# Kernel tuning notes

Hardware: AMD Instinct MI355X
Metric: run time of the kernel (lower is better)

The kernel has to match this reference:

```python
import jax, jax.numpy as jnp
import numpy as np

B, NPG, HID, HEADS, L = 8, 512, 128, 8, 4
N = B * NPG
E = 16384
EDIM = HID // 4  # edge_dim = hidden_dim // 4 = 32


def _ln(x, g, b):
    m = x.mean(-1, keepdims=True)
    v = ((x - m) ** 2).mean(-1, keepdims=True)
    return (x - m) / jnp.sqrt(v + 1e-5) * g + b


def setup_inputs() -> dict:
    key = jax.random.key(0)
    ks = jax.random.split(key, 24)
    s = 0.05
    epg = E // B
    base = jnp.repeat(jnp.arange(B) * NPG, epg)
    src = base + jax.random.randint(ks[0], (E,), 0, NPG)
    dst = base + jax.random.randint(ks[1], (E,), 0, NPG)
    d = {
        'x': jax.random.randint(ks[2], (N, 1), 0, 100),
        'edge_index': jnp.stack([src, dst]),
        'edge_attr': jax.random.normal(ks[3], (E, 1), jnp.float32),
        'batch': jnp.repeat(jnp.arange(B), NPG),
        'atom_emb': jax.random.normal(ks[4], (100, HID)) * s,
        'edge_w': jax.random.normal(ks[5], (1, EDIM)) * s,
        'edge_b': jnp.zeros((EDIM,)),
        'wq': jax.random.normal(ks[6], (L, HID, HEADS * HID)) * s,
        'bq': jnp.zeros((L, HEADS * HID)),
        'wk': jax.random.normal(ks[7], (L, HID, HEADS * HID)) * s,
        'bk': jnp.zeros((L, HEADS * HID)),
        'wv': jax.random.normal(ks[8], (L, HID, HEADS * HID)) * s,
        'bv': jnp.zeros((L, HEADS * HID)),
        'we': jax.random.normal(ks[9], (L, EDIM, HEADS * HID)) * s,
        'wskip': jax.random.normal(ks[10], (L, HID, HID)) * s,
        'bskip': jnp.zeros((L, HID)),
        'ln_g': jnp.ones((L, HID)),
        'ln_b': jnp.zeros((L, HID)),
        'mha_in_w': jax.random.normal(ks[11], (HID, 3 * HID)) * s,
        'mha_in_b': jnp.zeros((3 * HID,)),
        'mha_out_w': jax.random.normal(ks[12], (HID, HID)) * s,
        'mha_out_b': jnp.zeros((HID,)),
        'w1': jax.random.normal(ks[13], (HID, HID)) * s,
        'b1': jnp.zeros((HID,)),
        'w2': jax.random.normal(ks[14], (HID, HID // 2)) * s,
        'b2': jnp.zeros((HID // 2,)),
        'w3': jax.random.normal(ks[15], (HID // 2, 3)) * s,
        'b3': jnp.zeros((3,)),
    }
    return d


def reference(x, edge_index, edge_attr, batch, atom_emb, edge_w, edge_b,
              wq, bq, wk, bk, wv, bv, we, wskip, bskip, ln_g, ln_b,
              mha_in_w, mha_in_b, mha_out_w, mha_out_b, w1, b1, w2, b2, w3, b3):
    src, dst = edge_index[0], edge_index[1]
    h = atom_emb[x[:, 0]]                       # [N, HID]
    e = edge_attr @ edge_w + edge_b             # [E, EDIM]
    scale = 1.0 / jnp.sqrt(jnp.float32(HID))    # per-head channel dim = HID
    for i in range(L):
        res = h
        q = (h @ wq[i] + bq[i]).reshape(N, HEADS, HID)
        k = (h @ wk[i] + bk[i]).reshape(N, HEADS, HID)
        v = (h @ wv[i] + bv[i]).reshape(N, HEADS, HID)
        ee = (e @ we[i]).reshape(E, HEADS, HID)
        kj = k[src] + ee                        # [E, HEADS, HID]
        vj = v[src] + ee
        logits = jnp.einsum('ehd,ehd->eh', q[dst], kj) * scale
        m = jax.ops.segment_max(logits, dst, num_segments=N)
        a = jnp.exp(logits - m[dst])
        z = jax.ops.segment_sum(a, dst, num_segments=N)
        a = a / (z[dst] + 1e-16)                # edge softmax per target node
        agg = jax.ops.segment_sum(a[:, :, None] * vj, dst, num_segments=N)
        out = agg.mean(axis=1) + h @ wskip[i] + bskip[i]  # concat=False + root skip
        h = jax.nn.gelu(_ln(out + res, ln_g[i], ln_b[i]), approximate=False)
    # equal-size graphs: ragged->padded conversion is a plain reshape, no padding
    p = h.reshape(B, NPG, HID)
    qkv = p @ mha_in_w + mha_in_b               # [B, n, 3*HID]
    hd = HID // HEADS
    q, k, v = [t.reshape(B, NPG, HEADS, hd).transpose(0, 2, 1, 3)
               for t in jnp.split(qkv, 3, axis=-1)]
    att = jax.nn.softmax(jnp.einsum('bhqd,bhkd->bhqk', q, k) / jnp.sqrt(jnp.float32(hd)), axis=-1)
    o = jnp.einsum('bhqk,bhkd->bhqd', att, v).transpose(0, 2, 1, 3).reshape(B, NPG, HID)
    o = (o @ mha_out_w + mha_out_b).reshape(N, HID)
    y = jax.nn.gelu(o @ w1 + b1, approximate=False)
    y = jax.nn.gelu(y @ w2 + b2, approximate=False)
    return y @ w3 + b3                          # [N, 3]
```

## Files before the change

kernel.cpp:

```cpp
#include <hip/hip_runtime.h>
#include <hip/hip_bf16.h>
#include <math.h>

#define NN 4096
#define NE 16384
#define NLAYERS 4

#define WT_STRIDE 442368

typedef __attribute__((ext_vector_type(8))) short bf16x8;
typedef __attribute__((ext_vector_type(4))) float floatx4;

__device__ __forceinline__ float gelu_f(float x) {
  return 0.5f * x * (1.0f + erff(x * 0.70710678118654752440f));
}

__device__ __forceinline__ void bsplit(float a, unsigned short& hi, unsigned short& lo) {
  __hip_bfloat16 h16 = __float2bfloat16(a);
  hi = *(unsigned short*)&h16;
  const float r = a - __bfloat162float(h16);
  __hip_bfloat16 l16 = __float2bfloat16(r);
  lo = *(unsigned short*)&l16;
}

union F16U { float4 v4[4]; float f[16]; };

__global__ void k_init(const int* __restrict__ x, const float* __restrict__ atom_emb,
                       const float* __restrict__ edge_attr, const float* __restrict__ edge_w,
                       const float* __restrict__ edge_b, float* __restrict__ h,
                       float* __restrict__ ef, int* __restrict__ counts,
                       unsigned short* __restrict__ hhi, unsigned short* __restrict__ hlo) {
  const int idx = blockIdx.x * 256 + threadIdx.x;
  const float hv = atom_emb[x[idx >> 7] * 128 + (idx & 127)];
  h[idx] = hv;
  bsplit(hv, hhi[idx], hlo[idx]);
  ef[idx] = edge_attr[idx >> 5] * edge_w[idx & 31] + edge_b[idx & 31];
  if (idx < NN) counts[idx] = 0;
}

__global__ void k_hist(const int* __restrict__ eidx, int* __restrict__ counts) {
  const int e = blockIdx.x * 256 + threadIdx.x;
  if (e < NE) atomicAdd(&counts[eidx[NE + e]], 1);
}

__global__ void k_scan2(const int* __restrict__ counts, int* __restrict__ offs,
                        const int* __restrict__ eidx, int* __restrict__ elist) {
  __shared__ int tmp[1024];
  __shared__ int sheads[4096];
  const int t = threadIdx.x;
  const int c0 = counts[t*4], c1 = counts[t*4+1], c2 = counts[t*4+2], c3 = counts[t*4+3];
  const int s = c0 + c1 + c2 + c3;
  tmp[t] = s; __syncthreads();
  for (int off = 1; off < 1024; off <<= 1) {
    int v = (t >= off) ? tmp[t - off] : 0;
    __syncthreads();
    tmp[t] += v;
    __syncthreads();
  }
  int base = tmp[t] - s;
  offs[t*4]   = base;                sheads[t*4]   = base;
  offs[t*4+1] = base + c0;           sheads[t*4+1] = base + c0;
  offs[t*4+2] = base + c0 + c1;      sheads[t*4+2] = base + c0 + c1;
  offs[t*4+3] = base + c0 + c1 + c2; sheads[t*4+3] = base + c0 + c1 + c2;
  if (t == 1023) offs[NN] = tmp[1023];
  __syncthreads();
  for (int e = t; e < NE; e += 1024) {
    const int p = atomicAdd(&sheads[eidx[NE + e]], 1);
    elist[p] = e;
  }
}

__global__ __launch_bounds__(256) void k_wcvt(
    const float* __restrict__ wq, const float* __restrict__ wk,
    const float* __restrict__ wv, const float* __restrict__ wsk,
    unsigned short* __restrict__ wthi, unsigned short* __restrict__ wtlo) {
  const int z = blockIdx.z;
  const int layer = z >> 2, mat = z & 3;
  int NC; const float* W; int woff;
  if (mat == 0)      { NC = 1024; W = wq  + (size_t)layer * 131072; woff = 0; }
  else if (mat == 1) { NC = 1024; W = wk  + (size_t)layer * 131072; woff = 131072; }
  else if (mat == 2) { NC = 1024; W = wv  + (size_t)layer * 131072; woff = 262144; }
  else               { NC = 128;  W = wsk + (size_t)layer * 16384;  woff = 393216; }
  const int c0 = blockIdx.x * 64;
  if (c0 >= NC) return;
  const int k0 = blockIdx.y * 64;
  __shared__ unsigned short th[64][65], tl[64][65];
  const int t = threadIdx.x;
  for (int i = t; i < 4096; i += 256) {
    const int kk = i >> 6, c = i & 63;
    bsplit(W[(size_t)(k0 + kk) * NC + c0 + c], th[kk][c], tl[kk][c]);
  }
  __syncthreads();
  unsigned short* oh = wthi + (size_t)layer * WT_STRIDE + woff;
  unsigned short* ol = wtlo + (size_t)layer * WT_STRIDE + woff;
  for (int i = t; i < 4096; i += 256) {
    const int n = i >> 6, k = i & 63;
    oh[(size_t)(c0 + n) * 128 + k0 + k] = th[k][n];
    ol[(size_t)(c0 + n) * 128 + k0 + k] = tl[k][n];
  }
}

__global__ __launch_bounds__(256) void k_wqe(
    const float* __restrict__ wq, const float* __restrict__ bq,
    const float* __restrict__ we, unsigned short* __restrict__ wthi,
    unsigned short* __restrict__ wtlo, float* __restrict__ bqe) {
  const int layer = blockIdx.x >> 3, hh = blockIdx.x & 7;
  const float* wq_l = wq + (size_t)layer * 131072;
  const float* we_l = we + (size_t)layer * 32768;
  const float* bq_l = bq + (size_t)layer * 1024;
  __shared__ float wqS[128][132];
  __shared__ float weS[32][132];
  const int t = threadIdx.x;
  for (int i = t; i < 4096; i += 256) {
    const int d = i >> 5, dd4 = (i & 31) << 2;
    *(float4*)&wqS[d][dd4] = *(const float4*)&wq_l[(size_t)d * 1024 + hh * 128 + dd4];
  }
  for (int i = t; i < 1024; i += 256) {
    const int c = i >> 5, dd4 = (i & 31) << 2;
    *(float4*)&weS[c][dd4] = *(const float4*)&we_l[(size_t)c * 1024 + hh * 128 + dd4];
  }
  __syncthreads();
  const int d = t & 127, cg = t >> 7;
  float acc[16];
  #pragma unroll
  for (int cc = 0; cc < 16; cc++) acc[cc] = 0.f;
  for (int dd = 0; dd < 128; dd++) {
    const float a = wqS[d][dd];
    #pragma unroll
    for (int cc = 0; cc < 16; cc++)
      acc[cc] += a * weS[cg * 16 + cc][dd];
  }
  unsigned short* oh = wthi + (size_t)layer * WT_STRIDE + 409600;
  unsigned short* ol = wtlo + (size_t)layer * WT_STRIDE + 409600;
  #pragma unroll
  for (int cc = 0; cc < 16; cc++) {
    const int j = hh * 32 + cg * 16 + cc;
    unsigned short hi, lo;
    bsplit(acc[cc], hi, lo);
    oh[(size_t)j * 128 + d] = hi;
    ol[(size_t)j * 128 + d] = lo;
  }
  if (t < 32) {
    float s = 0.f;
    for (int dd = 0; dd < 128; dd++) s += bq_l[hh * 128 + dd] * weS[t][dd];
    bqe[layer * 256 + hh * 32 + t] = s;
  }
}

__global__ __launch_bounds__(256) void k_mfqkv(
    const unsigned short* __restrict__ hhi, const unsigned short* __restrict__ hlo,
    const unsigned short* __restrict__ wth, const unsigned short* __restrict__ wtl,
    const float* __restrict__ bq, const float* __restrict__ bk,
    const float* __restrict__ bv, const float* __restrict__ bsk,
    const float* __restrict__ bqe_l,
    float* __restrict__ qb, float* __restrict__ kb,
    float* __restrict__ vb, float* __restrict__ skb, float* __restrict__ qeb) {
  const int xb = blockIdx.x;
  int NC; const float* bias; float* C; int woff; int c0;
  if (xb < 16)      { NC = 1024; bias = bq;    C = qb;  woff = 0;      c0 = xb * 64; }
  else if (xb < 32) { NC = 1024; bias = bk;    C = kb;  woff = 131072; c0 = (xb-16) * 64; }
  else if (xb < 48) { NC = 1024; bias = bv;    C = vb;  woff = 262144; c0 = (xb-32) * 64; }
  else if (xb < 50) { NC = 128;  bias = bsk;   C = skb; woff = 393216; c0 = (xb-48) * 64; }
  else              { NC = 256;  bias = bqe_l; C = qeb; woff = 409600; c0 = (xb-50) * 64; }
  __shared__ unsigned short Ah[64][136], Al[64][136], Wh[64][136], Wl[64][136];
  const int t = threadIdx.x;
  const int n0 = blockIdx.y * 64;
  for (int i = t; i < 1024; i += 256) {
    const int r = i >> 4, c8 = (i & 15) << 3;
    *(uint4*)&Ah[r][c8] = *(const uint4*)&hhi[(size_t)(n0 + r) * 128 + c8];
    *(uint4*)&Al[r][c8] = *(const uint4*)&hlo[(size_t)(n0 + r) * 128 + c8];
    *(uint4*)&Wh[r][c8] = *(const uint4*)&wth[woff + (size_t)(c0 + r) * 128 + c8];
    *(uint4*)&Wl[r][c8] = *(const uint4*)&wtl[woff + (size_t)(c0 + r) * 128 + c8];
  }
  __syncthreads();
  const int w = t >> 6, l = t & 63;
  const int quad = l >> 4, lm = l & 15;
  floatx4 acc[4] = {{0.f,0.f,0.f,0.f},{0.f,0.f,0.f,0.f},{0.f,0.f,0.f,0.f},{0.f,0.f,0.f,0.f}};
  #pragma unroll
  for (int kc = 0; kc < 4; kc++) {
    const int ko = kc * 32 + quad * 8;
    const bf16x8 ah = *(const bf16x8*)&Ah[w * 16 + lm][ko];
    const bf16x8 al = *(const bf16x8*)&Al[w * 16 + lm][ko];
    #pragma unroll
    for (int ct = 0; ct < 4; ct++) {
      const bf16x8 bh = *(const bf16x8*)&Wh[ct * 16 + lm][ko];
      const bf16x8 bl = *(const bf16x8*)&Wl[ct * 16 + lm][ko];
      acc[ct] = __builtin_amdgcn_mfma_f32_16x16x32_bf16(ah, bh, acc[ct], 0, 0, 0);
      acc[ct] = __builtin_amdgcn_mfma_f32_16x16x32_bf16(ah, bl, acc[ct], 0, 0, 0);
      acc[ct] = __builtin_amdgcn_mfma_f32_16x16x32_bf16(al, bh, acc[ct], 0, 0, 0);
    }
  }
  #pragma unroll
  for (int ct = 0; ct < 4; ct++) {
    const int col = c0 + ct * 16 + lm;
    const float bb = bias[col];
    #pragma unroll
    for (int r = 0; r < 4; r++) {
      const int row = n0 + w * 16 + quad * 4 + r;
      C[(size_t)row * NC + col] = acc[ct][r] + bb;
    }
  }
}

__global__ __launch_bounds__(256) void k_gemm2(const float* __restrict__ A,
                                               const float* __restrict__ W,
                                               const float* __restrict__ bias,
                                               float* __restrict__ C, int NC, int gelu) {
  __shared__ float As[128][65];
  __shared__ float Ws[128][64];
  const int t = threadIdx.x;
  const int n0 = blockIdx.y * 64, c0 = blockIdx.x * 64;
  for (int i = t; i < 2048; i += 256) {
    const int r = i & 63, k4 = (i >> 6) << 2;
    const float4 a = *(const float4*)&A[(size_t)(n0 + r) * 128 + k4];
    As[k4+0][r] = a.x; As[k4+1][r] = a.y; As[k4+2][r] = a.z; As[k4+3][r] = a.w;
  }
  for (int i = t; i < 2048; i += 256) {
    const int kk = i >> 4, c4 = (i & 15) << 2;
    *(float4*)&Ws[kk][c4] = *(const float4*)&W[(size_t)kk * NC + c0 + c4];
  }
  __syncthreads();
  const int tr = (t >> 4) << 2;
  const int tc = (t & 15) << 2;
  float acc[4][4];
  #pragma unroll
  for (int i = 0; i < 4; i++)
    #pragma unroll
    for (int j = 0; j < 4; j++) acc[i][j] = 0.f;
  #pragma unroll 8
  for (int k = 0; k < 128; k++) {
    const float4 av = *(const float4*)&As[k][tr];
    const float4 wv = *(const float4*)&Ws[k][tc];
    acc[0][0] += av.x*wv.x; acc[0][1] += av.x*wv.y; acc[0][2] += av.x*wv.z; acc[0][3] += av.x*wv.w;
    acc[1][0] += av.y*wv.x; acc[1][1] += av.y*wv.y; acc[1][2] += av.y*wv.z; acc[1][3] += av.y*wv.w;
    acc[2][0] += av.z*wv.x; acc[2][1] += av.z*wv.y; acc[2][2] += av.z*wv.z; acc[2][3] += av.z*wv.w;
    acc[3][0] += av.w*wv.x; acc[3][1] += av.w*wv.y; acc[3][2] += av.w*wv.z; acc[3][3] += av.w*wv.w;
  }
  const float4 bb = *(const float4*)&bias[c0 + tc];
  #pragma unroll
  for (int i = 0; i < 4; i++) {
    float4 v;
    v.x = acc[i][0] + bb.x; v.y = acc[i][1] + bb.y;
    v.z = acc[i][2] + bb.z; v.w = acc[i][3] + bb.w;
    if (gelu) { v.x = gelu_f(v.x); v.y = gelu_f(v.y); v.z = gelu_f(v.z); v.w = gelu_f(v.w); }
    *(float4*)&C[(size_t)(n0 + tr + i) * NC + c0 + tc] = v;
  }
}

__global__ __launch_bounds__(256) void k_edgepost(
    const float* __restrict__ qb, const float* __restrict__ kb,
    const float* __restrict__ vb, const float* __restrict__ qe,
    const float* __restrict__ ef, const int* __restrict__ offs,
    const int* __restrict__ elist, const int* __restrict__ eidx,
    const float* __restrict__ we_l, const float* __restrict__ skb,
    const float* __restrict__ lng, const float* __restrict__ lnb,
    float* __restrict__ h,
    unsigned short* __restrict__ hhi, unsigned short* __restrict__ hlo) {
  __shared__ float Ss[4][256];
  __shared__ float Am[4][128];
  const int t = threadIdx.x;
  const int wid = t >> 6, lane = t & 63;
  const int n0 = (blockIdx.x & 7) * 512 + (blockIdx.x >> 3) * 4;
  const int n = n0 + wid;
  {
    const int hh = lane >> 3, s8 = lane & 7;
    const int d0 = hh * 128 + s8 * 16;
    F16U qv;
    {
      const float4* qp = (const float4*)(qb + (size_t)n * 1024 + d0);
      #pragma unroll
      for (int i = 0; i < 4; i++) qv.v4[i] = qp[i];
    }
    const float4 qe4 = *(const float4*)(qe + (size_t)n * 256 + hh * 32 + s8 * 4);
    float m = -INFINITY, z = 0.f;
    float acc[16];
    #pragma unroll
    for (int i = 0; i < 16; i++) acc[i] = 0.f;
    float sx = 0.f, sy = 0.f, sz = 0.f, sw = 0.f;
    const int e0 = offs[n], e1 = offs[n + 1];
    int ecur = 0, scur = 0;
    if (e0 < e1) { ecur = elist[e0]; scur = eidx[ecur]; }
    for (int tt = e0; tt < e1; tt++) {
      F16U kv, vv;
      {
        const float4* kp = (const float4*)(kb + (size_t)scur * 1024 + d0);
        const float4* vp = (const float4*)(vb + (size_t)scur * 1024 + d0);
        #pragma unroll
        for (int i = 0; i < 4; i++) { kv.v4[i] = kp[i]; vv.v4[i] = vp[i]; }
      }
      const float4 ef4 = *(const float4*)(ef + (size_t)ecur * 32 + s8 * 4);
      if (tt + 1 < e1) { ecur = elist[tt + 1]; scur = eidx[ecur]; }
      float p0 = qe4.x*ef4.x + qe4.y*ef4.y;
      float p1 = qe4.z*ef4.z + qe4.w*ef4.w;
      float p2 = 0.f, p3 = 0.f;
      #pragma unroll
      for (int i = 0; i < 4; i++) {
        p0 += qv.f[i]      * kv.f[i];
        p1 += qv.f[4 + i]  * kv.f[4 + i];
        p2 += qv.f[8 + i]  * kv.f[8 + i];
        p3 += qv.f[12 + i] * kv.f[12 + i];
      }
      float p = (p0 + p1) + (p2 + p3);
      p += __shfl_xor(p, 1);
      p += __shfl_xor(p, 2);
      p += __shfl_xor(p, 4);
      const float logit = p * 0.08838834764831845f;
      if (logit > m + 8.f) {
        const float f = __expf(m - logit);
        z *= f; sx *= f; sy *= f; sz *= f; sw *= f;
        #pragma unroll
        for (int i = 0; i < 16; i++) acc[i] *= f;
        m = logit;
      }
      const float w = __expf(logit - m);
      z += w;
      #pragma unroll
      for (int i = 0; i < 16; i++) acc[i] += w * vv.f[i];
      sx += w * ef4.x; sy += w * ef4.y;
      sz += w * ef4.z; sw += w * ef4.w;
    }
    const float inv = 1.f / (z + 1e-16f);
    *(float4*)&Ss[wid][hh * 32 + s8 * 4] =
        make_float4(sx * inv, sy * inv, sz * inv, sw * inv);
    F16U ov;
    #pragma unroll
    for (int i = 0; i < 16; i++) ov.f[i] = acc[i] * inv;
    #pragma unroll
    for (int mask = 8; mask <= 32; mask <<= 1)
      #pragma unroll
      for (int i = 0; i < 16; i++) ov.f[i] += __shfl_xor(ov.f[i], mask);
    if (hh == 0) {
      #pragma unroll
      for (int i = 0; i < 16; i++) ov.f[i] *= 0.125f;
      #pragma unroll
      for (int i = 0; i < 4; i++)
        *(float4*)&Am[wid][s8 * 16 + i * 4] = ov.v4[i];
    }
  }
  {
    const int half = lane >> 5;
    const int q4 = (lane & 31) << 2;
    float ax = 0.f, ay = 0.f, az = 0.f, aw = 0.f;
    #pragma unroll 8
    for (int i = 0; i < 128; i++) {
      const int k = half * 128 + i;
      const float4 wv = *(const float4*)&we_l[(size_t)(k & 31) * 1024 + (k >> 5) * 128 + q4];
      const float s = Ss[wid][k];
      ax += s * wv.x; ay += s * wv.y; az += s * wv.z; aw += s * wv.w;
    }
    ax += __shfl_xor(ax, 32); ay += __shfl_xor(ay, 32);
    az += __shfl_xor(az, 32); aw += __shfl_xor(aw, 32);
    if (lane < 32) {
      const size_t o = (size_t)n * 128 + q4;
      const float4 sk4 = *(const float4*)&skb[o];
      const float4 h4  = *(const float4*)&h[o];
      float4 am = *(float4*)&Am[wid][q4];
      am.x += 0.125f * ax + sk4.x + h4.x;
      am.y += 0.125f * ay + sk4.y + h4.y;
      am.z += 0.125f * az + sk4.z + h4.z;
      am.w += 0.125f * aw + sk4.w + h4.w;
      *(float4*)&Am[wid][q4] = am;
    }
  }
  {
    const float v0 = Am[wid][lane], v1 = Am[wid][lane + 64];
    float s = v0 + v1;
    #pragma unroll
    for (int mask = 1; mask <= 32; mask <<= 1) s += __shfl_xor(s, mask);
    const float mean = s * (1.f / 128.f);
    const float d0 = v0 - mean, d1 = v1 - mean;
    float q = d0 * d0 + d1 * d1;
    #pragma unroll
    for (int mask = 1; mask <= 32; mask <<= 1) q += __shfl_xor(q, mask);
    const float rstd = 1.f / sqrtf(q * (1.f / 128.f) + 1e-5f);
    const float y0 = d0 * rstd * lng[lane] + lnb[lane];
    const float y1 = d1 * rstd * lng[lane + 64] + lnb[lane + 64];
    const float r0 = gelu_f(y0);
    const float r1 = gelu_f(y1);
    const size_t o = (size_t)n * 128 + lane;
    h[o] = r0;
    h[o + 64] = r1;
    bsplit(r0, hhi[o], hlo[o]);
    bsplit(r1, hhi[o + 64], hlo[o + 64]);
  }
}

__global__ __launch_bounds__(256) void k_attn2b(const float* __restrict__ qkvm,
                                                float* __restrict__ pm,
                                                float* __restrict__ pz,
                                                float* __restrict__ pacc) {
  __shared__ float ks2[64][16];
  __shared__ float vs2[64][16];
  const int ksp = blockIdx.x, qt = blockIdx.y, bh = blockIdx.z;
  const int b = bh >> 3, hh = bh & 7;
  const int t = threadIdx.x;
  const size_t rbase = (size_t)(b * 512 + ksp * 64);
  {
    const int j = t >> 2, d4 = (t & 3) << 2;
    const size_t ro = (rbase + j) * 384 + hh * 16 + d4;
    *(float4*)&ks2[j][d4] = *(const float4*)&qkvm[ro + 128];
    *(float4*)&vs2[j][d4] = *(const float4*)&qkvm[ro + 256];
  }
  __syncthreads();
  const int qrow = qt * 256 + t;
  const int nq = b * 512 + qrow;
  F16U qv;
  {
    const float4* qp = (const float4*)(qkvm + (size_t)nq * 384 + hh * 16);
    #pragma unroll
    for (int i = 0; i < 4; i++) qv.v4[i] = qp[i];
  }
  float m = -INFINITY, z = 0.f;
  float acc[16];
  #pragma unroll
  for (int i = 0; i < 16; i++) acc[i] = 0.f;
  for (int j = 0; j < 64; j += 2) {
    F16U k0, k1, v0, v1;
    {
      const float4* p0 = (const float4*)ks2[j];
      const float4* p1 = (const float4*)ks2[j + 1];
      const float4* q0 = (const float4*)vs2[j];
      const float4* q1 = (const float4*)vs2[j + 1];
      #pragma unroll
      for (int i = 0; i < 4; i++) {
        k0.v4[i] = p0[i]; k1.v4[i] = p1[i];
        v0.v4[i] = q0[i]; v1.v4[i] = q1[i];
      }
    }
    float a0 = 0.f, a1 = 0.f, a2 = 0.f, a3 = 0.f;
    float b0 = 0.f, b1 = 0.f, b2 = 0.f, b3 = 0.f;
    #pragma unroll
    for (int i = 0; i < 4; i++) {
      a0 += qv.f[i]      * k0.f[i];
      a1 += qv.f[4 + i]  * k0.f[4 + i];
      a2 += qv.f[8 + i]  * k0.f[8 + i];
      a3 += qv.f[12 + i] * k0.f[12 + i];
      b0 += qv.f[i]      * k1.f[i];
      b1 += qv.f[4 + i]  * k1.f[4 + i];
      b2 += qv.f[8 + i]  * k1.f[8 + i];
      b3 += qv.f[12 + i] * k1.f[12 + i];
    }
    const float sa = ((a0 + a1) + (a2 + a3)) * 0.25f;
    const float sb = ((b0 + b1) + (b2 + b3)) * 0.25f;
    const float smax = fmaxf(sa, sb);
    if (smax > m + 8.f) {
      const float f = __expf(m - smax);
      z *= f;
      #pragma unroll
      for (int i = 0; i < 16; i++) acc[i] *= f;
      m = smax;
    }
    const float wa = __expf(sa - m);
    const float wb = __expf(sb - m);
    z += wa + wb;
    #pragma unroll
    for (int i = 0; i < 16; i++)
      acc[i] += wa * v0.f[i] + wb * v1.f[i];
  }
  const int p = (bh * 512 + qrow) * 8 + ksp;
  pm[p] = m; pz[p] = z;
  float4* pp = (float4*)&pacc[(size_t)p * 16];
  F16U ov;
  #pragma unroll
  for (int i = 0; i < 16; i++) ov.f[i] = acc[i];
  #pragma unroll
  for (int i = 0; i < 4; i++) pp[i] = ov.v4[i];
}

__global__ __launch_bounds__(256) void k_tail(
    const float* __restrict__ pm, const float* __restrict__ pz,
    const float* __restrict__ pacc,
    const float* __restrict__ mow, const float* __restrict__ mob,
    const float* __restrict__ w1, const float* __restrict__ b1,
    const float* __restrict__ w2, const float* __restrict__ b2,
    const float* __restrict__ w3, const float* __restrict__ b3,
    float* __restrict__ out) {
  __shared__ float RA[8][128];
  __shared__ float RB[8][128];
  const int t = threadIdx.x;
  const int w = t >> 6, lane = t & 63;
  const int n0 = blockIdx.x * 8;
  const int rA = w * 2, rB = w * 2 + 1;
  #pragma unroll
  for (int rr = 0; rr < 2; rr++) {
    const int n = n0 + w * 2 + rr;
    const int b = n >> 9, qrow = n & 511;
    #pragma unroll
    for (int half = 0; half < 2; half++) {
      const int c = lane + half * 64;
      const int hh = c >> 4, d = c & 15;
      const int base = ((b * 8 + hh) * 512 + qrow) * 8;
      float ms = pm[base];
      #pragma unroll
      for (int s = 1; s < 8; s++) ms = fmaxf(ms, pm[base + s]);
      float z = 0.f, o = 0.f;
      #pragma unroll
      for (int s = 0; s < 8; s++) {
        const float wg = __expf(pm[base + s] - ms);
        z += pz[base + s] * wg;
        o += pacc[(size_t)(base + s) * 16 + d] * wg;
      }
      RA[w * 2 + rr][c] = o / z;
    }
  }
  {
    const int kk = lane >> 5;
    const int c4 = (lane & 31) << 2;
    float a0x=0.f,a0y=0.f,a0z=0.f,a0w=0.f, a1x=0.f,a1y=0.f,a1z=0.f,a1w=0.f;
    #pragma unroll 8
    for (int i = 0; i < 64; i++) {
      const int k = kk + (i << 1);
      const float4 wv = *(const float4*)&mow[(size_t)k * 128 + c4];
      const float r0 = RA[rA][k], r1 = RA[rB][k];
      a0x += r0*wv.x; a0y += r0*wv.y; a0z += r0*wv.z; a0w += r0*wv.w;
      a1x += r1*wv.x; a1y += r1*wv.y; a1z += r1*wv.z; a1w += r1*wv.w;
    }
    a0x += __shfl_xor(a0x, 32); a0y += __shfl_xor(a0y, 32);
    a0z += __shfl_xor(a0z, 32); a0w += __shfl_xor(a0w, 32);
    a1x += __shfl_xor(a1x, 32); a1y += __shfl_xor(a1y, 32);
    a1z += __shfl_xor(a1z, 32); a1w += __shfl_xor(a1w, 32);
    if (lane < 32) {
      RB[rA][c4+0] = a0x + mob[c4+0]; RB[rA][c4+1] = a0y + mob[c4+1];
      RB[rA][c4+2] = a0z + mob[c4+2]; RB[rA][c4+3] = a0w + mob[c4+3];
      RB[rB][c4+0] = a1x + mob[c4+0]; RB[rB][c4+1] = a1y + mob[c4+1];
      RB[rB][c4+2] = a1z + mob[c4+2]; RB[rB][c4+3] = a1w + mob[c4+3];
    }
  }
  {
    const int kk = lane >> 5;
    const int c4 = (lane & 31) << 2;
    float a0x=0.f,a0y=0.f,a0z=0.f,a0w=0.f, a1x=0.f,a1y=0.f,a1z=0.f,a1w=0.f;
    #pragma unroll 8
    for (int i = 0; i < 64; i++) {
      const int k = kk + (i << 1);
      const float4 wv = *(const float4*)&w1[(size_t)k * 128 + c4];
      const float r0 = RB[rA][k], r1 = RB[rB][k];
      a0x += r0*wv.x; a0y += r0*wv.y; a0z += r0*wv.z; a0w += r0*wv.w;
      a1x += r1*wv.x; a1y += r1*wv.y; a1z += r1*wv.z; a1w += r1*wv.w;
    }
    a0x += __shfl_xor(a0x, 32); a0y += __shfl_xor(a0y, 32);
    a0z += __shfl_xor(a0z, 32); a0w += __shfl_xor(a0w, 32);
    a1x += __shfl_xor(a1x, 32); a1y += __shfl_xor(a1y, 32);
    a1z += __shfl_xor(a1z, 32); a1w += __shfl_xor(a1w, 32);
    if (lane < 32) {
      RA[rA][c4+0] = gelu_f(a0x + b1[c4+0]); RA[rA][c4+1] = gelu_f(a0y + b1[c4+1]);
      RA[rA][c4+2] = gelu_f(a0z + b1[c4+2]); RA[rA][c4+3] = gelu_f(a0w + b1[c4+3]);
      RB[rA][c4+0] = 0.f;
      RA[rB][c4+0] = gelu_f(a1x + b1[c4+0]); RA[rB][c4+1] = gelu_f(a1y + b1[c4+1]);
      RA[rB][c4+2] = gelu_f(a1z + b1[c4+2]); RA[rB][c4+3] = gelu_f(a1w + b1[c4+3]);
    }
  }
  {
    const int kk = lane >> 4;
    const int c4 = (lane & 15) << 2;
    float a0x=0.f,a0y=0.f,a0z=0.f,a0w=0.f, a1x=0.f,a1y=0.f,a1z=0.f,a1w=0.f;
    #pragma unroll 8
    for (int i = 0; i < 32; i++) {
      const int k = kk + (i << 2);
      const float4 wv = *(const float4*)&w2[(size_t)k * 64 + c4];
      const float r0 = RA[rA][k], r1 = RA[rB][k];
      a0x += r0*wv.x; a0y += r0*wv.y; a0z += r0*wv.z; a0w += r0*wv.w;
      a1x += r1*wv.x; a1y += r1*wv.y; a1z += r1*wv.z; a1w += r1*wv.w;
    }
    a0x += __shfl_xor(a0x, 16); a0y += __shfl_xor(a0y, 16);
    a0z += __shfl_xor(a0z, 16); a0w += __shfl_xor(a0w, 16);
    a1x += __shfl_xor(a1x, 16); a1y += __shfl_xor(a1y, 16);
    a1z += __shfl_xor(a1z, 16); a1w += __shfl_xor(a1w, 16);
    a0x += __shfl_xor(a0x, 32); a0y += __shfl_xor(a0y, 32);
    a0z += __shfl_xor(a0z, 32); a0w += __shfl_xor(a0w, 32);
    a1x += __shfl_xor(a1x, 32); a1y += __shfl_xor(a1y, 32);
    a1z += __shfl_xor(a1z, 32); a1w += __shfl_xor(a1w, 32);
    if (lane < 16) {
      RB[rA][c4+0] = gelu_f(a0x + b2[c4+0]); RB[rA][c4+1] = gelu_f(a0y + b2[c4+1]);
      RB[rA][c4+2] = gelu_f(a0z + b2[c4+2]); RB[rA][c4+3] = gelu_f(a0w + b2[c4+3]);
      RB[rB][c4+0] = gelu_f(a1x + b2[c4+0]); RB[rB][c4+1] = gelu_f(a1y + b2[c4+1]);
      RB[rB][c4+2] = gelu_f(a1z + b2[c4+2]); RB[rB][c4+3] = gelu_f(a1w + b2[c4+3]);
    }
  }
  if (lane < 3) {
    #pragma unroll
    for (int rr = 0; rr < 2; rr++) {
      const int row = w * 2 + rr;
      float s = b3[lane];
      for (int c = 0; c < 64; c++) s += RB[row][c] * w3[c * 3 + lane];
      out[(size_t)(n0 + row) * 3 + lane] = s;
    }
  }
}

extern "C" void kernel_launch(void* const* d_in, const int* in_sizes, int n_in,
                              void* d_out, int out_size, void* d_ws, size_t ws_size,
                              hipStream_t stream) {
  const int*   x         = (const int*)d_in[0];
  const int*   eidx      = (const int*)d_in[1];
  const float* edge_attr = (const float*)d_in[2];
  const float* atom_emb  = (const float*)d_in[4];
  const float* edge_w    = (const float*)d_in[5];
  const float* edge_b    = (const float*)d_in[6];
  const float* wq        = (const float*)d_in[7];
  const float* bq        = (const float*)d_in[8];
  const float* wk        = (const float*)d_in[9];
  const float* bk        = (const float*)d_in[10];
  const float* wv        = (const float*)d_in[11];
  const float* bv        = (const float*)d_in[12];
  const float* we        = (const float*)d_in[13];
  const float* wskip     = (const float*)d_in[14];
  const float* bskip     = (const float*)d_in[15];
  const float* ln_g      = (const float*)d_in[16];
  const float* ln_b      = (const float*)d_in[17];
  const float* mha_in_w  = (const float*)d_in[18];
  const float* mha_in_b  = (const float*)d_in[19];
  const float* mha_out_w = (const float*)d_in[20];
  const float* mha_out_b = (const float*)d_in[21];
  const float* w1        = (const float*)d_in[22];
  const float* b1        = (const float*)d_in[23];
  const float* w2        = (const float*)d_in[24];
  const float* b2        = (const float*)d_in[25];
  const float* w3        = (const float*)d_in[26];
  const float* b3        = (const float*)d_in[27];

  float* ws   = (float*)d_ws;
  float* h    = ws;
  float* ef   = h + 524288;
  float* qb   = ef + 524288;
  float* kb   = qb + 4194304;
  float* vb   = kb + 4194304;
  float* qe   = vb + 4194304;
  float* big  = qe + 1048576;
  float* skb  = big + 1048576;
  unsigned short* hhi  = (unsigned short*)(big + 1572864);
  unsigned short* hlo  = hhi + 524288;
  unsigned short* wthi = hlo + 524288;
  unsigned short* wtlo = wthi + 1769472;
  float* sbuf = big + 4194304;
  float* qkvm = qb;
  float* pm   = sbuf;
  float* pz   = sbuf + 262144;
  float* pacc = big;
  int* counts = (int*)(sbuf + 1048576);
  int* offs   = counts + 4100;
  int* heads  = offs + 4100;
  int* elist  = heads + 4100;
  float* bqe  = (float*)(elist + 16384);

  k_init<<<2048, 256, 0, stream>>>(x, atom_emb, edge_attr, edge_w, edge_b, h, ef, counts,
                                   hhi, hlo);
  k_hist<<<64, 256, 0, stream>>>(eidx, counts);
  k_scan2<<<1, 1024, 0, stream>>>(counts, offs, eidx, elist);
  k_wcvt<<<dim3(16, 2, 16), 256, 0, stream>>>(wq, wk, wv, wskip, wthi, wtlo);
  k_wqe<<<32, 256, 0, stream>>>(wq, bq, we, wthi, wtlo, bqe);

  for (int i = 0; i < NLAYERS; i++) {
    const float* bq_i  = bq + (size_t)i * 1024;
    const float* bk_i  = bk + (size_t)i * 1024;
    const float* bv_i  = bv + (size_t)i * 1024;
    const float* we_i  = we + (size_t)i * 32768;
    const float* bsk_i = bskip + (size_t)i * 128;
    const float* g_i   = ln_g + (size_t)i * 128;
    const float* b_i   = ln_b + (size_t)i * 128;
    const unsigned short* wth_i = wthi + (size_t)i * WT_STRIDE;
    const unsigned short* wtl_i = wtlo + (size_t)i * WT_STRIDE;

    k_mfqkv<<<dim3(54, 64), 256, 0, stream>>>(hhi, hlo, wth_i, wtl_i,
                                              bq_i, bk_i, bv_i, bsk_i, bqe + i * 256,
                                              qb, kb, vb, skb, qe);
    k_edgepost<<<1024, 256, 0, stream>>>(qb, kb, vb, qe, ef, offs, elist, eidx,
                                         we_i, skb, g_i, b_i, h, hhi, hlo);
  }

  k_gemm2<<<dim3(6, 64), 256, 0, stream>>>(h, mha_in_w, mha_in_b, qkvm, 384, 0);
  k_attn2b<<<dim3(8, 2, 64), 256, 0, stream>>>(qkvm, pm, pz, pacc);
  k_tail<<<512, 256, 0, stream>>>(pm, pz, pacc,
                                  mha_out_w, mha_out_b, w1, b1, w2, b2, w3, b3,
                                  (float*)d_out);
}
```

Before: 454.6 us.

## Split each node's edge loop across two waves and merge softmax partials

k_edgepost now launches 512 threads per block so two wavefronts share each target node, each walking every other incoming edge with its own online-softmax state. The odd wave writes its running max, sum and accumulators to shared memory, and the even wave rescales and merges them before the existing projection, layernorm and GELU epilogue. This halves the serial chain of dependent gather loads per wave and raises memory-level parallelism. The cost is extra shared memory, a block barrier, and half the waves sitting idle after the merge. A stray store that zeroed RB in k_tail is also removed.

```diff
diff --git a/kernel.cpp b/kernel.cpp
--- a/kernel.cpp
+++ b/kernel.cpp
@@ -247,7 +247,7 @@
   }
 }
 
-__global__ __launch_bounds__(256) void k_edgepost(
+__global__ __launch_bounds__(512) void k_edgepost(
     const float* __restrict__ qb, const float* __restrict__ kb,
     const float* __restrict__ vb, const float* __restrict__ qe,
     const float* __restrict__ ef, const int* __restrict__ offs,
@@ -258,13 +258,22 @@
     unsigned short* __restrict__ hhi, unsigned short* __restrict__ hlo) {
   __shared__ float Ss[4][256];
   __shared__ float Am[4][128];
+  __shared__ float Pacc[4][64][16];
+  __shared__ float Psv[4][64][4];
+  __shared__ float Pmz[4][2];
   const int t = threadIdx.x;
   const int wid = t >> 6, lane = t & 63;
+  const int p = wid >> 1, par = wid & 1;
   const int n0 = (blockIdx.x & 7) * 512 + (blockIdx.x >> 3) * 4;
-  const int n = n0 + wid;
-  {
-    const int hh = lane >> 3, s8 = lane & 7;
-    const int d0 = hh * 128 + s8 * 16;
+  const int n = n0 + p;
+  const int hh = lane >> 3, s8 = lane & 7;
+  const int d0 = hh * 128 + s8 * 16;
+  float m = -INFINITY, z = 0.f;
+  float acc[16];
+  #pragma unroll
+  for (int i = 0; i < 16; i++) acc[i] = 0.f;
+  float sx = 0.f, sy = 0.f, sz = 0.f, sw = 0.f;
+  {
     F16U qv;
     {
       const float4* qp = (const float4*)(qb + (size_t)n * 1024 + d0);
@@ -272,15 +281,11 @@
       for (int i = 0; i < 4; i++) qv.v4[i] = qp[i];
     }
     const float4 qe4 = *(const float4*)(qe + (size_t)n * 256 + hh * 32 + s8 * 4);
-    float m = -INFINITY, z = 0.f;
-    float acc[16];
-    #pragma unroll
-    for (int i = 0; i < 16; i++) acc[i] = 0.f;
-    float sx = 0.f, sy = 0.f, sz = 0.f, sw = 0.f;
     const int e0 = offs[n], e1 = offs[n + 1];
+    int tt = e0 + par;
     int ecur = 0, scur = 0;
-    if (e0 < e1) { ecur = elist[e0]; scur = eidx[ecur]; }
-    for (int tt = e0; tt < e1; tt++) {
+    if (tt < e1) { ecur = elist[tt]; scur = eidx[ecur]; }
+    for (; tt < e1; tt += 2) {
       F16U kv, vv;
       {
         const float4* kp = (const float4*)(kb + (size_t)scur * 1024 + d0);
@@ -289,7 +294,7 @@
         for (int i = 0; i < 4; i++) { kv.v4[i] = kp[i]; vv.v4[i] = vp[i]; }
       }
       const float4 ef4 = *(const float4*)(ef + (size_t)ecur * 32 + s8 * 4);
-      if (tt + 1 < e1) { ecur = elist[tt + 1]; scur = eidx[ecur]; }
+      if (tt + 2 < e1) { ecur = elist[tt + 2]; scur = eidx[ecur]; }
       float p0 = qe4.x*ef4.x + qe4.y*ef4.y;
       float p1 = qe4.z*ef4.z + qe4.w*ef4.w;
       float p2 = 0.f, p3 = 0.f;
@@ -300,11 +305,11 @@
         p2 += qv.f[8 + i]  * kv.f[8 + i];
         p3 += qv.f[12 + i] * kv.f[12 + i];
       }
-      float p = (p0 + p1) + (p2 + p3);
-      p += __shfl_xor(p, 1);
-      p += __shfl_xor(p, 2);
-      p += __shfl_xor(p, 4);
-      const float logit = p * 0.08838834764831845f;
+      float pp = (p0 + p1) + (p2 + p3);
+      pp += __shfl_xor(pp, 1);
+      pp += __shfl_xor(pp, 2);
+      pp += __shfl_xor(pp, 4);
+      const float logit = pp * 0.08838834764831845f;
       if (logit > m + 8.f) {
         const float f = __expf(m - logit);
         z *= f; sx *= f; sy *= f; sz *= f; sw *= f;
@@ -319,8 +324,32 @@
       sx += w * ef4.x; sy += w * ef4.y;
       sz += w * ef4.z; sw += w * ef4.w;
     }
+  }
+  if (par == 1) {
+    #pragma unroll
+    for (int i = 0; i < 16; i++) Pacc[p][lane][i] = acc[i];
+    Psv[p][lane][0] = sx; Psv[p][lane][1] = sy;
+    Psv[p][lane][2] = sz; Psv[p][lane][3] = sw;
+    if (lane == 0) { Pmz[p][0] = m; Pmz[p][1] = z; }
+  }
+  __syncthreads();
+  if (par == 1) return;
+  {
+    const float mB = Pmz[p][0], zB = Pmz[p][1];
+    const float mstar = fmaxf(m, mB);
+    const float fA = (z  > 0.f) ? __expf(m  - mstar) : 0.f;
+    const float fB = (zB > 0.f) ? __expf(mB - mstar) : 0.f;
+    z = z * fA + zB * fB;
+    #pragma unroll
+    for (int i = 0; i < 16; i++) acc[i] = acc[i] * fA + Pacc[p][lane][i] * fB;
+    sx = sx * fA + Psv[p][lane][0] * fB;
+    sy = sy * fA + Psv[p][lane][1] * fB;
+    sz = sz * fA + Psv[p][lane][2] * fB;
+    sw = sw * fA + Psv[p][lane][3] * fB;
+  }
+  {
     const float inv = 1.f / (z + 1e-16f);
-    *(float4*)&Ss[wid][hh * 32 + s8 * 4] =
+    *(float4*)&Ss[p][hh * 32 + s8 * 4] =
         make_float4(sx * inv, sy * inv, sz * inv, sw * inv);
     F16U ov;
     #pragma unroll
@@ -334,7 +363,7 @@
       for (int i = 0; i < 16; i++) ov.f[i] *= 0.125f;
       #pragma unroll
       for (int i = 0; i < 4; i++)
-        *(float4*)&Am[wid][s8 * 16 + i * 4] = ov.v4[i];
+        *(float4*)&Am[p][s8 * 16 + i * 4] = ov.v4[i];
     }
   }
   {
@@ -345,7 +374,7 @@
     for (int i = 0; i < 128; i++) {
       const int k = half * 128 + i;
       const float4 wv = *(const float4*)&we_l[(size_t)(k & 31) * 1024 + (k >> 5) * 128 + q4];
-      const float s = Ss[wid][k];
+      const float s = Ss[p][k];
       ax += s * wv.x; ay += s * wv.y; az += s * wv.z; aw += s * wv.w;
     }
     ax += __shfl_xor(ax, 32); ay += __shfl_xor(ay, 32);
@@ -354,27 +383,27 @@
       const size_t o = (size_t)n * 128 + q4;
       const float4 sk4 = *(const float4*)&skb[o];
       const float4 h4  = *(const float4*)&h[o];
-      float4 am = *(float4*)&Am[wid][q4];
+      float4 am = *(float4*)&Am[p][q4];
       am.x += 0.125f * ax + sk4.x + h4.x;
       am.y += 0.125f * ay + sk4.y + h4.y;
       am.z += 0.125f * az + sk4.z + h4.z;
       am.w += 0.125f * aw + sk4.w + h4.w;
-      *(float4*)&Am[wid][q4] = am;
-    }
-  }
-  {
-    const float v0 = Am[wid][lane], v1 = Am[wid][lane + 64];
+      *(float4*)&Am[p][q4] = am;
+    }
+  }
+  {
+    const float v0 = Am[p][lane], v1 = Am[p][lane + 64];
     float s = v0 + v1;
     #pragma unroll
     for (int mask = 1; mask <= 32; mask <<= 1) s += __shfl_xor(s, mask);
     const float mean = s * (1.f / 128.f);
-    const float d0 = v0 - mean, d1 = v1 - mean;
-    float q = d0 * d0 + d1 * d1;
+    const float d0v = v0 - mean, d1v = v1 - mean;
+    float q = d0v * d0v + d1v * d1v;
     #pragma unroll
     for (int mask = 1; mask <= 32; mask <<= 1) q += __shfl_xor(q, mask);
     const float rstd = 1.f / sqrtf(q * (1.f / 128.f) + 1e-5f);
-    const float y0 = d0 * rstd * lng[lane] + lnb[lane];
-    const float y1 = d1 * rstd * lng[lane + 64] + lnb[lane + 64];
+    const float y0 = d0v * rstd * lng[lane] + lnb[lane];
+    const float y1 = d1v * rstd * lng[lane + 64] + lnb[lane + 64];
     const float r0 = gelu_f(y0);
     const float r1 = gelu_f(y1);
     const size_t o = (size_t)n * 128 + lane;
@@ -545,7 +574,6 @@
     if (lane < 32) {
       RA[rA][c4+0] = gelu_f(a0x + b1[c4+0]); RA[rA][c4+1] = gelu_f(a0y + b1[c4+1]);
       RA[rA][c4+2] = gelu_f(a0z + b1[c4+2]); RA[rA][c4+3] = gelu_f(a0w + b1[c4+3]);
-      RB[rA][c4+0] = 0.f;
       RA[rB][c4+0] = gelu_f(a1x + b1[c4+0]); RA[rB][c4+1] = gelu_f(a1y + b1[c4+1]);
       RA[rB][c4+2] = gelu_f(a1z + b1[c4+2]); RA[rB][c4+3] = gelu_f(a1w + b1[c4+3]);
     }
@@ -664,7 +692,7 @@
     k_mfqkv<<<dim3(54, 64), 256, 0, stream>>>(hhi, hlo, wth_i, wtl_i,
                                               bq_i, bk_i, bv_i, bsk_i, bqe + i * 256,
                                               qb, kb, vb, skb, qe);
-    k_edgepost<<<1024, 256, 0, stream>>>(qb, kb, vb, qe, ef, offs, elist, eidx,
+    k_edgepost<<<1024, 512, 0, stream>>>(qb, kb, vb, qe, ef, offs, elist, eidx,
                                          we_i, skb, g_i, b_i, h, hhi, hlo);
   }
 
```

Result: slower. 468.6 us (+3.1%).
